# Optimization experiments

Hardware: AMD Instinct MI355X
Metric: run time of the kernel (lower is better)

Reference implementation:

```python
import jax, jax.numpy as jnp
import numpy as np

N = 50000      # nodes
E = 625000     # edges
D_IN = 128     # in_feats
D_OUT = 128    # out_feats


def setup_inputs() -> dict:
    key = jax.random.key(0)
    k1, k2, k3, k4, k5, k6 = jax.random.split(key, 6)
    feat = jax.random.normal(k1, (N, D_IN), dtype=jnp.float32)
    affine = jax.random.uniform(k2, (E,), dtype=jnp.float32)
    src = jax.random.randint(k3, (E,), 0, N, dtype=jnp.int32)
    dst = jnp.sort(jax.random.randint(k4, (E,), 0, N, dtype=jnp.int32))
    # Linear(in_feats*2, out_feats): torch stores weight [out, in]; use [in, out] here
    bound = 1.0 / np.sqrt(2 * D_IN)
    W = jax.random.uniform(k5, (2 * D_IN, D_OUT), minval=-bound, maxval=bound, dtype=jnp.float32)
    b = jax.random.uniform(k6, (D_OUT,), minval=-bound, maxval=bound, dtype=jnp.float32)
    return {"feat": feat, "affine": affine, "src": src, "dst": dst, "W": W, "b": b}


def reference(feat, affine, src, dst, W, b):
    # u_mul_e: per-edge message = srcfeat[src] * edge scalar 'affine'
    msg = feat[src] * affine[:, None]                      # [E, D_IN]
    # fn.sum: scatter-add messages to destination nodes
    agg = jax.ops.segment_sum(msg, dst, num_segments=N)    # [N, D_IN]
    # concat dst features with aggregated neighborhood, then linear
    gcn_feat = jnp.concatenate([feat, agg], axis=-1)       # [N, 2*D_IN]
    return gcn_feat @ W + b                                # [N, D_OUT]
```

## Files before the change

### kernel.cpp

```cpp
#include <hip/hip_runtime.h>

#define N_NODES 50000
#define E_EDGES 625000
#define D 128

typedef __attribute__((ext_vector_type(8)))  short  short8;
typedef __attribute__((ext_vector_type(16))) float  floatx16;

static __device__ inline unsigned short f2bf(float f) {
    union { float f; unsigned u; } v; v.f = f;
    unsigned r = v.u + 0x7FFFu + ((v.u >> 16) & 1u);
    return (unsigned short)(r >> 16);
}
static __device__ inline float bflo(unsigned p) { return __uint_as_float(p << 16); }
static __device__ inline float bfhi(unsigned p) { return __uint_as_float(p & 0xFFFF0000u); }

__global__ __launch_bounds__(256) void prep_kernel(const int* __restrict__ dst,
                                                   const float* __restrict__ W,
                                                   const int* __restrict__ src,
                                                   const float* __restrict__ affine,
                                                   int* __restrict__ rowptr,
                                                   unsigned short* __restrict__ wimg,
                                                   uint2* __restrict__ meta) {
    int t = blockIdx.x * 256 + threadIdx.x;
    if (t < E_EDGES) {
        int d1 = dst[t];
        int d0 = (t == 0) ? -1 : dst[t - 1];
        for (int n = d0 + 1; n <= d1; ++n) rowptr[n] = t;
        if (t == E_EDGES - 1)
            for (int n = d1 + 1; n <= N_NODES; ++n) rowptr[n] = E_EDGES;
        uint2 m;
        m.x = (unsigned)src[t];
        m.y = __float_as_uint(affine[t]);
        meta[t] = m;
    }
    if (t < 4096) {
        int n = t & 127;
        int c = (t >> 7) & 15;
        int h = t >> 11;
        int krow = h * 128 + c * 8;
        short8 v;
        #pragma unroll
        for (int j = 0; j < 8; ++j)
            v[j] = (short)f2bf(W[(size_t)(krow + j) * D + n]);
        *((short8*)wimg + t) = v;
    }
}

#define NB_M 391

__global__ __launch_bounds__(256, 3) void gemm_mfma(const float* __restrict__ feat,
                                                    const unsigned short* __restrict__ wimg,
                                                    unsigned short* __restrict__ Z1b,
                                                    unsigned short* __restrict__ Y) {
    __shared__ short8 Bls[2048];

    int tid = threadIdx.x;
    int idx = blockIdx.x;
    int h   = (idx >> 3) & 1;
    int b   = ((idx >> 4) << 3) | (idx & 7);
    if (b >= NB_M) return;

    const short8* wsrc = (const short8*)wimg + h * 2048;
    #pragma unroll
    for (int i = 0; i < 8; ++i)
        Bls[tid + i * 256] = wsrc[tid + i * 256];

    int wave = tid >> 6;
    int lane = tid & 63;
    int m = lane & 31;
    int g = lane >> 5;
    int row0   = b * 128 + wave * 32;
    int row_a  = row0 + m;
    int rclamp = row_a < N_NODES ? row_a : 0;

    short8 fa[8];
    const float* ap = feat + (size_t)rclamp * D + g * 8;
    #pragma unroll
    for (int ks = 0; ks < 8; ++ks) {
        float4 u = *(const float4*)(ap + ks * 16);
        float4 v = *(const float4*)(ap + ks * 16 + 4);
        short8 a;
        a[0] = (short)f2bf(u.x); a[1] = (short)f2bf(u.y);
        a[2] = (short)f2bf(u.z); a[3] = (short)f2bf(u.w);
        a[4] = (short)f2bf(v.x); a[5] = (short)f2bf(v.y);
        a[6] = (short)f2bf(v.z); a[7] = (short)f2bf(v.w);
        fa[ks] = a;
    }
    __syncthreads();

    unsigned short* dstbuf = h ? Y : Z1b;

    #pragma unroll
    for (int t4 = 0; t4 < 4; ++t4) {
        int n = t4 * 32 + m;
        floatx16 acc = {0,0,0,0, 0,0,0,0, 0,0,0,0, 0,0,0,0};
        #pragma unroll
        for (int ks = 0; ks < 8; ++ks) {
            short8 bb = Bls[(ks * 2 + g) * 128 + n];
            acc = __builtin_amdgcn_mfma_f32_32x32x16_bf16(fa[ks], bb, acc, 0, 0, 0);
        }
        #pragma unroll
        for (int r = 0; r < 16; ++r) {
            int row = row0 + (r & 3) + 8 * (r >> 2) + 4 * g;
            if (row < N_NODES) dstbuf[(size_t)row * D + n] = f2bf(acc[r]);
        }
    }
}

__global__ __launch_bounds__(256) void agg_add(const unsigned short* __restrict__ Y,
                                               const unsigned short* __restrict__ Z1b,
                                               const uint2* __restrict__ meta,
                                               const int* __restrict__ rowptr,
                                               const float* __restrict__ bias,
                                               float* __restrict__ out) {
    int wave = threadIdx.x >> 6;
    int lane = threadIdx.x & 63;
    int n = blockIdx.x * 4 + wave;
    if (n >= N_NODES) return;
    int lo = rowptr[n], hi = rowptr[n + 1];
    int g  = lane >> 4;
    int jj = (lane & 15) << 3;
    const unsigned short* Yj = Y + jj;

    uint4  z  = *(const uint4*)(Z1b + (size_t)n * D + jj);
    float4 b0 = *(const float4*)(bias + jj);
    float4 b1 = *(const float4*)(bias + jj + 4);

    float acc[8] = {0,0,0,0,0,0,0,0};

    for (int e0 = lo; e0 < hi; e0 += 16) {
        uint2 md[4];
        #pragma unroll
        for (int u = 0; u < 4; ++u) {
            int i = e0 + u * 4 + g;
            md[u] = meta[i < hi ? i : lo];
        }
        float w[4];
        uint4 p[4];
        #pragma unroll
        for (int u = 0; u < 4; ++u) {
            int i = e0 + u * 4 + g;
            w[u] = (i < hi) ? __uint_as_float(md[u].y) : 0.f;
            p[u] = *(const uint4*)(Yj + (size_t)md[u].x * D);
        }
        #pragma unroll
        for (int u = 0; u < 4; ++u) {
            acc[0] += bflo(p[u].x) * w[u];  acc[1] += bfhi(p[u].x) * w[u];
            acc[2] += bflo(p[u].y) * w[u];  acc[3] += bfhi(p[u].y) * w[u];
            acc[4] += bflo(p[u].z) * w[u];  acc[5] += bfhi(p[u].z) * w[u];
            acc[6] += bflo(p[u].w) * w[u];  acc[7] += bfhi(p[u].w) * w[u];
        }
    }

    #pragma unroll
    for (int r = 0; r < 8; ++r) {
        acc[r] += __shfl_xor(acc[r], 16);
        acc[r] += __shfl_xor(acc[r], 32);
    }

    if (g == 0) {
        float* op = out + (size_t)n * D + jj;
        float4 o0, o1;
        o0.x = bflo(z.x) + b0.x + acc[0];  o0.y = bfhi(z.x) + b0.y + acc[1];
        o0.z = bflo(z.y) + b0.z + acc[2];  o0.w = bfhi(z.y) + b0.w + acc[3];
        o1.x = bflo(z.z) + b1.x + acc[4];  o1.y = bfhi(z.z) + b1.y + acc[5];
        o1.z = bflo(z.w) + b1.z + acc[6];  o1.w = bfhi(z.w) + b1.w + acc[7];
        *(float4*)op       = o0;
        *(float4*)(op + 4) = o1;
    }
}

extern "C" void kernel_launch(void* const* d_in, const int* in_sizes, int n_in,
                              void* d_out, int out_size, void* d_ws, size_t ws_size,
                              hipStream_t stream) {
    const float* feat   = (const float*)d_in[0];
    const float* affine = (const float*)d_in[1];
    const int*   src    = (const int*)  d_in[2];
    const int*   dst    = (const int*)  d_in[3];
    const float* W      = (const float*)d_in[4];
    const float* bias   = (const float*)d_in[5];
    float*       out    = (float*)d_out;

    unsigned short* wimg   = (unsigned short*)d_ws;
    int*            rowptr = (int*)((char*)d_ws + 65536);
    uint2*          meta   = (uint2*)((char*)d_ws + 266240);
    unsigned short* Y      = (unsigned short*)((char*)d_ws + 5267456);
    unsigned short* Z1b    = (unsigned short*)((char*)d_ws + 18067456);

    prep_kernel<<<(E_EDGES + 255) / 256, 256, 0, stream>>>(dst, W, src, affine,
                                                           rowptr, wimg, meta);
    int gemm_blocks = ((2 * NB_M + 15) / 16) * 16;
    gemm_mfma<<<gemm_blocks, 256, 0, stream>>>(feat, wimg, Z1b, Y);
    agg_add<<<(N_NODES + 3) / 4, 256, 0, stream>>>(Y, Z1b, meta, rowptr, bias, out);
}
```

Baseline: 126.2 us.

## Replace rowptr/meta prep pass with in-kernel binary search over sorted dst

Drops the edge-wide prep pass that built the CSR row pointers and packed (src, affine) metadata, keeping only a small weight-conversion kernel. The aggregation kernel now finds each block's edge range with a binary search over the sorted dst array and reads src and affine directly. This removes one full pass over the edge arrays plus the metadata writes, at the cost of a per-block binary search, a block barrier, and two separate gathers per edge instead of one packed load.

```diff
diff --git a/kernel.cpp b/kernel.cpp
--- a/kernel.cpp
+++ b/kernel.cpp
@@ -15,36 +15,18 @@
 static __device__ inline float bflo(unsigned p) { return __uint_as_float(p << 16); }
 static __device__ inline float bfhi(unsigned p) { return __uint_as_float(p & 0xFFFF0000u); }
 
-__global__ __launch_bounds__(256) void prep_kernel(const int* __restrict__ dst,
-                                                   const float* __restrict__ W,
-                                                   const int* __restrict__ src,
-                                                   const float* __restrict__ affine,
-                                                   int* __restrict__ rowptr,
-                                                   unsigned short* __restrict__ wimg,
-                                                   uint2* __restrict__ meta) {
+__global__ __launch_bounds__(256) void prep_w(const float* __restrict__ W,
+                                              unsigned short* __restrict__ wimg) {
     int t = blockIdx.x * 256 + threadIdx.x;
-    if (t < E_EDGES) {
-        int d1 = dst[t];
-        int d0 = (t == 0) ? -1 : dst[t - 1];
-        for (int n = d0 + 1; n <= d1; ++n) rowptr[n] = t;
-        if (t == E_EDGES - 1)
-            for (int n = d1 + 1; n <= N_NODES; ++n) rowptr[n] = E_EDGES;
-        uint2 m;
-        m.x = (unsigned)src[t];
-        m.y = __float_as_uint(affine[t]);
-        meta[t] = m;
-    }
-    if (t < 4096) {
-        int n = t & 127;
-        int c = (t >> 7) & 15;
-        int h = t >> 11;
-        int krow = h * 128 + c * 8;
-        short8 v;
-        #pragma unroll
-        for (int j = 0; j < 8; ++j)
-            v[j] = (short)f2bf(W[(size_t)(krow + j) * D + n]);
-        *((short8*)wimg + t) = v;
-    }
+    int n = t & 127;
+    int c = (t >> 7) & 15;
+    int h = t >> 11;
+    int krow = h * 128 + c * 8;
+    short8 v;
+    #pragma unroll
+    for (int j = 0; j < 8; ++j)
+        v[j] = (short)f2bf(W[(size_t)(krow + j) * D + n]);
+    *((short8*)wimg + t) = v;
 }
 
 #define NB_M 391
@@ -110,15 +92,30 @@
 
 __global__ __launch_bounds__(256) void agg_add(const unsigned short* __restrict__ Y,
                                                const unsigned short* __restrict__ Z1b,
-                                               const uint2* __restrict__ meta,
-                                               const int* __restrict__ rowptr,
+                                               const int* __restrict__ src,
+                                               const float* __restrict__ affine,
+                                               const int* __restrict__ dst,
                                                const float* __restrict__ bias,
                                                float* __restrict__ out) {
-    int wave = threadIdx.x >> 6;
-    int lane = threadIdx.x & 63;
-    int n = blockIdx.x * 4 + wave;
-    if (n >= N_NODES) return;
-    int lo = rowptr[n], hi = rowptr[n + 1];
+    __shared__ int bnd[5];
+    int tid = threadIdx.x;
+    int n_base = blockIdx.x * 4;
+
+    if (tid < 5) {
+        int target = n_base + tid;
+        int lo = 0, hi = E_EDGES;
+        while (lo < hi) {
+            int mid = (lo + hi) >> 1;
+            if (dst[mid] < target) lo = mid + 1; else hi = mid;
+        }
+        bnd[tid] = lo;
+    }
+    __syncthreads();
+
+    int wave = tid >> 6;
+    int lane = tid & 63;
+    int n = n_base + wave;
+    int lo = bnd[wave], hi = bnd[wave + 1];
     int g  = lane >> 4;
     int jj = (lane & 15) << 3;
     const unsigned short* Yj = Y + jj;
@@ -130,20 +127,20 @@
     float acc[8] = {0,0,0,0,0,0,0,0};
 
     for (int e0 = lo; e0 < hi; e0 += 16) {
-        uint2 md[4];
+        int   sidx[4];
+        float w[4];
         #pragma unroll
         for (int u = 0; u < 4; ++u) {
-            int i = e0 + u * 4 + g;
-            md[u] = meta[i < hi ? i : lo];
+            int  i = e0 + u * 4 + g;
+            bool v = i < hi;
+            int ic = v ? i : lo;
+            sidx[u] = src[ic];
+            w[u]    = v ? affine[ic] : 0.f;
         }
-        float w[4];
         uint4 p[4];
         #pragma unroll
-        for (int u = 0; u < 4; ++u) {
-            int i = e0 + u * 4 + g;
-            w[u] = (i < hi) ? __uint_as_float(md[u].y) : 0.f;
-            p[u] = *(const uint4*)(Yj + (size_t)md[u].x * D);
-        }
+        for (int u = 0; u < 4; ++u)
+            p[u] = *(const uint4*)(Yj + (size_t)sidx[u] * D);
         #pragma unroll
         for (int u = 0; u < 4; ++u) {
             acc[0] += bflo(p[u].x) * w[u];  acc[1] += bfhi(p[u].x) * w[u];
@@ -182,15 +179,12 @@
     const float* bias   = (const float*)d_in[5];
     float*       out    = (float*)d_out;
 
-    unsigned short* wimg   = (unsigned short*)d_ws;
-    int*            rowptr = (int*)((char*)d_ws + 65536);
-    uint2*          meta   = (uint2*)((char*)d_ws + 266240);
-    unsigned short* Y      = (unsigned short*)((char*)d_ws + 5267456);
-    unsigned short* Z1b    = (unsigned short*)((char*)d_ws + 18067456);
+    unsigned short* wimg = (unsigned short*)d_ws;
+    unsigned short* Y    = (unsigned short*)((char*)d_ws + 65536);
+    unsigned short* Z1b  = (unsigned short*)((char*)d_ws + 12865536);
 
-    prep_kernel<<<(E_EDGES + 255) / 256, 256, 0, stream>>>(dst, W, src, affine,
-                                                           rowptr, wimg, meta);
+    prep_w<<<16, 256, 0, stream>>>(W, wimg);
     int gemm_blocks = ((2 * NB_M + 15) / 16) * 16;
     gemm_mfma<<<gemm_blocks, 256, 0, stream>>>(feat, wimg, Z1b, Y);
-    agg_add<<<(N_NODES + 3) / 4, 256, 0, stream>>>(Y, Z1b, meta, rowptr, bias, out);
+    agg_add<<<N_NODES / 4, 256, 0, stream>>>(Y, Z1b, src, affine, dst, bias, out);
 }
```

Measured after the change: 157.9 us. +25.2%, slower.

## Fold edge CSR/meta construction into GEMM kernel, shrink weight prep kernel

Applied to the files above, without the earlier changes.

Moves the rowptr and packed (src, affine) meta construction out of the large prep kernel and into the start of the GEMM kernel: each of the 800 GEMM blocks handles a contiguous chunk of edges before its MFMA work. The prep kernel now only converts W to bf16 with 16 blocks. The goal is to cut one large launch and overlap the memory-bound edge preprocessing with the compute-bound GEMM. In exchange, GEMM blocks do extra serial work before their matrix math, which may lengthen the GEMM kernel.

```diff
diff --git a/kernel.cpp b/kernel.cpp
--- a/kernel.cpp
+++ b/kernel.cpp
@@ -3,6 +3,9 @@
 #define N_NODES 50000
 #define E_EDGES 625000
 #define D 128
+#define NB_M 391
+#define GEMM_BLOCKS 800
+#define EPB 782
 
 typedef __attribute__((ext_vector_type(8)))  short  short8;
 typedef __attribute__((ext_vector_type(16))) float  floatx16;
@@ -15,50 +18,52 @@
 static __device__ inline float bflo(unsigned p) { return __uint_as_float(p << 16); }
 static __device__ inline float bfhi(unsigned p) { return __uint_as_float(p & 0xFFFF0000u); }
 
-__global__ __launch_bounds__(256) void prep_kernel(const int* __restrict__ dst,
-                                                   const float* __restrict__ W,
-                                                   const int* __restrict__ src,
-                                                   const float* __restrict__ affine,
-                                                   int* __restrict__ rowptr,
-                                                   unsigned short* __restrict__ wimg,
-                                                   uint2* __restrict__ meta) {
+__global__ __launch_bounds__(256) void prep_w(const float* __restrict__ W,
+                                              unsigned short* __restrict__ wimg) {
     int t = blockIdx.x * 256 + threadIdx.x;
-    if (t < E_EDGES) {
-        int d1 = dst[t];
-        int d0 = (t == 0) ? -1 : dst[t - 1];
-        for (int n = d0 + 1; n <= d1; ++n) rowptr[n] = t;
-        if (t == E_EDGES - 1)
-            for (int n = d1 + 1; n <= N_NODES; ++n) rowptr[n] = E_EDGES;
-        uint2 m;
-        m.x = (unsigned)src[t];
-        m.y = __float_as_uint(affine[t]);
-        meta[t] = m;
-    }
-    if (t < 4096) {
-        int n = t & 127;
-        int c = (t >> 7) & 15;
-        int h = t >> 11;
-        int krow = h * 128 + c * 8;
-        short8 v;
-        #pragma unroll
-        for (int j = 0; j < 8; ++j)
-            v[j] = (short)f2bf(W[(size_t)(krow + j) * D + n]);
-        *((short8*)wimg + t) = v;
-    }
-}
-
-#define NB_M 391
+    int n = t & 127;
+    int c = (t >> 7) & 15;
+    int h = t >> 11;
+    int krow = h * 128 + c * 8;
+    short8 v;
+    #pragma unroll
+    for (int j = 0; j < 8; ++j)
+        v[j] = (short)f2bf(W[(size_t)(krow + j) * D + n]);
+    *((short8*)wimg + t) = v;
+}
 
 __global__ __launch_bounds__(256, 3) void gemm_mfma(const float* __restrict__ feat,
                                                     const unsigned short* __restrict__ wimg,
+                                                    const int* __restrict__ src,
+                                                    const int* __restrict__ dst,
+                                                    const float* __restrict__ affine,
+                                                    int* __restrict__ rowptr,
+                                                    uint2* __restrict__ meta,
                                                     unsigned short* __restrict__ Z1b,
                                                     unsigned short* __restrict__ Y) {
     __shared__ short8 Bls[2048];
 
     int tid = threadIdx.x;
     int idx = blockIdx.x;
-    int h   = (idx >> 3) & 1;
-    int b   = ((idx >> 4) << 3) | (idx & 7);
+
+    {
+        int e0 = idx * EPB;
+        int e1 = e0 + EPB; if (e1 > E_EDGES) e1 = E_EDGES;
+        for (int e = e0 + tid; e < e1; e += 256) {
+            int d1 = dst[e];
+            int d0 = (e == 0) ? -1 : dst[e - 1];
+            for (int n = d0 + 1; n <= d1; ++n) rowptr[n] = e;
+            if (e == E_EDGES - 1)
+                for (int n = d1 + 1; n <= N_NODES; ++n) rowptr[n] = E_EDGES;
+            uint2 m;
+            m.x = (unsigned)src[e];
+            m.y = __float_as_uint(affine[e]);
+            meta[e] = m;
+        }
+    }
+
+    int h = (idx >> 3) & 1;
+    int b = ((idx >> 4) << 3) | (idx & 7);
     if (b >= NB_M) return;
 
     const short8* wsrc = (const short8*)wimg + h * 2048;
@@ -188,9 +193,8 @@
     unsigned short* Y      = (unsigned short*)((char*)d_ws + 5267456);
     unsigned short* Z1b    = (unsigned short*)((char*)d_ws + 18067456);
 
-    prep_kernel<<<(E_EDGES + 255) / 256, 256, 0, stream>>>(dst, W, src, affine,
-                                                           rowptr, wimg, meta);
-    int gemm_blocks = ((2 * NB_M + 15) / 16) * 16;
-    gemm_mfma<<<gemm_blocks, 256, 0, stream>>>(feat, wimg, Z1b, Y);
+    prep_w<<<16, 256, 0, stream>>>(W, wimg);
+    gemm_mfma<<<GEMM_BLOCKS, 256, 0, stream>>>(feat, wimg, src, dst, affine,
+                                               rowptr, meta, Z1b, Y);
     agg_add<<<(N_NODES + 3) / 4, 256, 0, stream>>>(Y, Z1b, meta, rowptr, bias, out);
 }
```

New measurement: 127.3 us. Within noise of the previous version (+0.9%).
